# Kernel tuning notes

Hardware: AMD Instinct MI355X
Metric: run time of the kernel (lower is better)

The kernel has to match this reference:

```python
import jax, jax.numpy as jnp
import numpy as np

N_EMBD = 1024
N_HEAD = 16


def setup_inputs() -> dict:
    key = jax.random.key(0)
    k1, k2, k3, k4, k5 = jax.random.split(key, 5)
    B, T, C = 4, 2048, N_EMBD
    s = 1.0 / np.sqrt(C)
    x = jax.random.normal(k1, (B, T, C), dtype=jnp.float32)
    w_weight = jax.random.normal(k2, (3 * C, C), dtype=jnp.float32) * s
    w_bias = jax.random.normal(k3, (3 * C,), dtype=jnp.float32) * s
    proj_weight = jax.random.normal(k4, (C, C), dtype=jnp.float32) * s
    proj_bias = jax.random.normal(k5, (C,), dtype=jnp.float32) * s
    return {"x": x, "w_weight": w_weight, "w_bias": w_bias,
            "proj_weight": proj_weight, "proj_bias": proj_bias}


def reference(x, w_weight, w_bias, proj_weight, proj_bias):
    B, T, C = x.shape
    nh = N_HEAD
    hs = C // nh
    # fused QKV projection (torch Linear: x @ W^T + b)
    wei = jnp.einsum('btc,oc->bto', x, w_weight) + w_bias
    k, q, v = jnp.split(wei, 3, axis=-1)  # note: chunk order is k, q, v
    # [B, T, nh, hs] -> [B, nh, T, hs]
    key_ = k.reshape(B, T, nh, hs).transpose(0, 2, 1, 3)
    query = q.reshape(B, T, nh, hs).transpose(0, 2, 1, 3)
    value = v.reshape(B, T, nh, hs).transpose(0, 2, 1, 3)
    scale = hs ** (-0.5)
    weight = jnp.einsum('bhqd,bhkd->bhqk', query, key_) * scale
    weight = jax.nn.softmax(weight, axis=-1)
    out = jnp.einsum('bhqk,bhkd->bhqd', weight, value)  # [B, nh, T, hs]
    # Faithful to source bug: transpose(1,2) is discarded; view is taken on
    # the (B, nh, T, hs) layout directly.
    out = out.reshape(B, T, C)
    out = jnp.einsum('btc,oc->bto', out, proj_weight) + proj_bias
    return out
```

## Files before the change

kernel.cpp:

```cpp
#include <hip/hip_runtime.h>
#include <hip/hip_bf16.h>


typedef __attribute__((ext_vector_type(8)))  short bf16x8;
typedef __attribute__((ext_vector_type(4)))  float f32x4;
typedef __attribute__((ext_vector_type(16))) float f32x16;
typedef __attribute__((ext_vector_type(2)))  unsigned u32x2;

typedef __attribute__((address_space(3))) unsigned lds_u32_t;
typedef __attribute__((address_space(1))) unsigned glb_u32_t;

__device__ __forceinline__ void async_cp16(const short* g, short* l) {
    __builtin_amdgcn_global_load_lds((glb_u32_t*)g, (lds_u32_t*)l, 16, 0, 0);
}

__device__ __forceinline__ float exp2fast(float x) {
    return __builtin_amdgcn_exp2f(x);
}

__device__ __forceinline__ short f2bf(float f) {
    union { float f; unsigned u; } v; v.f = f;
    unsigned r = v.u + 0x7fffu + ((v.u >> 16) & 1u);
    return (short)(r >> 16);
}

__device__ __forceinline__ unsigned cvt_pk_bf16(float lo, float hi) {
    unsigned r;
    asm("v_cvt_pk_bf16_f32 %0, %1, %2" : "=v"(r) : "v"(lo), "v"(hi));
    return r;
}

__global__ __launch_bounds__(256) void cvt3_kernel(
    const float4* __restrict__ x,  const float4* __restrict__ ww,
    const float4* __restrict__ pw, short4* __restrict__ xb,
    short4* __restrict__ wwb,      short4* __restrict__ pwb) {
    const int b = blockIdx.x;
    const float4* in; short4* out; int i;
    if (b < 8192)       { in = x;  out = xb;  i = b * 256 + threadIdx.x; }
    else if (b < 11264) { in = ww; out = wwb; i = (b - 8192) * 256 + threadIdx.x; }
    else                { in = pw; out = pwb; i = (b - 11264) * 256 + threadIdx.x; }
    float4 v = in[i];
    short4 o;
    o.x = f2bf(v.x); o.y = f2bf(v.y); o.z = f2bf(v.z); o.w = f2bf(v.w);
    out[i] = o;
}

template<int EPI>
__global__ __launch_bounds__(256) void gemm_bf16(
    const short* __restrict__ A, const short* __restrict__ W,
    const float* __restrict__ bias, float* __restrict__ outF,
    short* __restrict__ kout, short* __restrict__ qout, short* __restrict__ vtout,
    int M, int N, int K)
{
    __shared__ short lA[2][128 * 64];
    __shared__ short lB[2][128 * 64];
    const int tid  = threadIdx.x;
    const int lane = tid & 63;
    const int wave = tid >> 6;
    const int wM = (wave >> 1) * 64;
    const int wN = (wave & 1) * 64;
    const int l15 = lane & 15, l4 = lane >> 4;
    const int rsw = (lane & 7) << 3;
    const int rowBase = blockIdx.y * 128;
    const int colBase = blockIdx.x * 128;

    auto STAGE = [&](int t, int buf) {
        const int k0 = t * 64;
        #pragma unroll
        for (int i = 0; i < 4; ++i) {
            int idx = i * 256 + tid;
            int r   = idx >> 3;
            int cp  = ((idx & 7) ^ (r & 7)) * 8;
            int eo  = idx * 8;
            async_cp16(A + (size_t)(rowBase + r) * K + k0 + cp, &lA[buf][eo]);
            async_cp16(W + (size_t)(colBase + r) * K + k0 + cp, &lB[buf][eo]);
        }
    };

    f32x4 acc[4][4] = {};
    const int NT = K >> 6;

    STAGE(0, 0);
    __syncthreads();

    int cur = 0;
    for (int t = 0; t < NT; ++t) {
        if (t + 1 < NT) STAGE(t + 1, cur ^ 1);
        #pragma unroll
        for (int kt = 0; kt < 2; ++kt) {
            bf16x8 af[4], bfr[4];
            #pragma unroll
            for (int mt = 0; mt < 4; ++mt)
                af[mt] = *(const bf16x8*)(
                    &lA[cur][(wM + mt * 16 + l15) * 64 + ((kt * 32 + l4 * 8) ^ rsw)]);
            #pragma unroll
            for (int nt = 0; nt < 4; ++nt)
                bfr[nt] = *(const bf16x8*)(
                    &lB[cur][(wN + nt * 16 + l15) * 64 + ((kt * 32 + l4 * 8) ^ rsw)]);
            #pragma unroll
            for (int mt = 0; mt < 4; ++mt)
                #pragma unroll
                for (int nt = 0; nt < 4; ++nt)
                    acc[mt][nt] = __builtin_amdgcn_mfma_f32_16x16x32_bf16(
                        af[mt], bfr[nt], acc[mt][nt], 0, 0, 0);
        }
        __syncthreads();
        cur ^= 1;
    }

    #pragma unroll
    for (int mt = 0; mt < 4; ++mt) {
        #pragma unroll
        for (int nt = 0; nt < 4; ++nt) {
            const int n  = colBase + wN + nt * 16 + l15;
            const int mb = rowBase + wM + mt * 16 + l4 * 4;
            const float bv = bias[n];
            #pragma unroll
            for (int r = 0; r < 4; ++r) {
                const int m = mb + r;
                float val = acc[mt][nt][r] + bv;
                if (EPI == 0) {
                    int b = m >> 11, t = m & 2047;
                    int j = n >> 10, hd = n & 1023;
                    int h = hd >> 6, d = hd & 63;
                    size_t base = ((size_t)(b * 16 + h) * 2048 + t) * 64 + d;
                    if (j == 0)      kout[base] = f2bf(val);
                    else if (j == 1) qout[base] = f2bf(val * 0.180336879f);
                    else             vtout[((size_t)(b * 16 + h) * 64 + d) * 2048 + t] = f2bf(val);
                } else {
                    outF[(size_t)m * N + n] = val;
                }
            }
        }
    }
}

__global__ __launch_bounds__(256) void attn_kernel(
    const short* __restrict__ Q, const short* __restrict__ Km,
    const short* __restrict__ Vt, short* __restrict__ O)
{
    __shared__ short kbuf[2][64 * 64];
    __shared__ short vbuf[2][64 * 64];

    const int tid  = threadIdx.x;
    const int lane = tid & 63;
    const int wave = tid >> 6;
    const int l31 = lane & 31;
    const int l1  = lane >> 5;

    const int b     = blockIdx.x;
    const int xcd   = b & 7;
    const int inner = b >> 3;
    const int bx    = inner & 15;
    const int bh    = xcd * 8 + (inner >> 4);
    const int q0    = bx * 128 + wave * 32;

    const short* Qh = Q  + (size_t)bh * 2048 * 64;
    const short* Kh = Km + (size_t)bh * 2048 * 64;
    const short* Vh = Vt + (size_t)bh * 64 * 2048;

    const int i8 = lane >> 3, i7 = lane & 7;
    const int srcCol = 8 * (i7 ^ i8);
    const int rsw    = (l31 & 7) << 3;

    const short* src[4];
    short* dst0[4];
    int step;
    if (wave < 2) {
        #pragma unroll
        for (int c = 0; c < 4; ++c) {
            int j = wave * 4 + c;
            src[c]  = Kh + (size_t)(8 * j + i8) * 64 + srcCol;
            dst0[c] = &kbuf[0][j * 512 + lane * 8];
        }
        step = 64 * 64;
    } else {
        #pragma unroll
        for (int c = 0; c < 4; ++c) {
            int j = (wave - 2) * 4 + c;
            src[c]  = Vh + (size_t)(8 * j + i8) * 2048 + srcCol;
            dst0[c] = &vbuf[0][j * 512 + lane * 8];
        }
        step = 64;
    }
    auto STAGE = [&](int buf) {
        #pragma unroll
        for (int c = 0; c < 4; ++c) {
            async_cp16(src[c], dst0[c] + buf * 4096);
            src[c] += step;
        }
    };

    bf16x8 qf[4];
    #pragma unroll
    for (int s = 0; s < 4; ++s)
        qf[s] = *(const bf16x8*)(Qh + (size_t)(q0 + l31) * 64 + s * 16 + l1 * 8);

    union { unsigned u[4]; bf16x8 v; } onesu;
    #pragma unroll
    for (int j = 0; j < 4; ++j) onesu.u[j] = 0x3F803F80u;
    const bf16x8 onesf = onesu.v;

    f32x16 o[2] = {};
    f32x16 ol   = {};

    STAGE(0);
    __syncthreads();

    int cur = 0;
    for (int it = 0; it < 32; ++it) {
        if (it < 31) STAGE(cur ^ 1);

        f32x16 s2[2] = {};
        __builtin_amdgcn_s_setprio(1);
        #pragma unroll
        for (int t = 0; t < 2; ++t) {
            #pragma unroll
            for (int s = 0; s < 4; ++s) {
                bf16x8 kf = *(const bf16x8*)(
                    &kbuf[cur][(t * 32 + l31) * 64 + ((s * 16 + l1 * 8) ^ rsw)]);
                s2[t] = __builtin_amdgcn_mfma_f32_32x32x16_bf16(kf, qf[s], s2[t], 0, 0, 0);
            }
        }
        __builtin_amdgcn_s_setprio(0);

        #pragma unroll
        for (int t = 0; t < 2; ++t)
            #pragma unroll
            for (int i = 0; i < 16; ++i)
                s2[t][i] = exp2fast(s2[t][i]);

        bf16x8 pa[4];
        #pragma unroll
        for (int t = 0; t < 2; ++t) {
            #pragma unroll
            for (int sl = 0; sl < 2; ++sl) {
                unsigned A0 = cvt_pk_bf16(s2[t][8 * sl + 0], s2[t][8 * sl + 1]);
                unsigned A1 = cvt_pk_bf16(s2[t][8 * sl + 2], s2[t][8 * sl + 3]);
                unsigned B0 = cvt_pk_bf16(s2[t][8 * sl + 4], s2[t][8 * sl + 5]);
                unsigned B1 = cvt_pk_bf16(s2[t][8 * sl + 6], s2[t][8 * sl + 7]);
                u32x2 ra = __builtin_amdgcn_permlane32_swap(A0, B0, false, false);
                u32x2 rb = __builtin_amdgcn_permlane32_swap(A1, B1, false, false);
                union { unsigned u[4]; bf16x8 v; } w;
                w.u[0] = ra.x;
                w.u[1] = rb.x;
                w.u[2] = ra.y;
                w.u[3] = rb.y;
                pa[2 * t + sl] = w.v;
            }
        }

        __builtin_amdgcn_s_setprio(1);
        #pragma unroll
        for (int s = 0; s < 4; ++s) {
            #pragma unroll
            for (int dt = 0; dt < 2; ++dt) {
                bf16x8 vf = *(const bf16x8*)(
                    &vbuf[cur][(dt * 32 + l31) * 64 + ((s * 16 + l1 * 8) ^ rsw)]);
                o[dt] = __builtin_amdgcn_mfma_f32_32x32x16_bf16(pa[s], vf, o[dt], 0, 0, 0);
            }
            ol = __builtin_amdgcn_mfma_f32_32x32x16_bf16(pa[s], onesf, ol, 0, 0, 0);
        }
        __builtin_amdgcn_s_setprio(0);

        __syncthreads();
        cur ^= 1;
    }

    #pragma unroll
    for (int g = 0; g < 4; ++g)
        #pragma unroll
        for (int rr = 0; rr < 4; ++rr) {
            float invl = 1.f / ol[g * 4 + rr];
            int qrow = q0 + rr + 8 * g + 4 * l1;
            size_t base = ((size_t)bh * 2048 + qrow) * 64 + l31;
            O[base]      = f2bf(o[0][g * 4 + rr] * invl);
            O[base + 32] = f2bf(o[1][g * 4 + rr] * invl);
        }
}

extern "C" void kernel_launch(void* const* d_in, const int* in_sizes, int n_in,
                              void* d_out, int out_size, void* d_ws, size_t ws_size,
                              hipStream_t stream) {
    const float* x  = (const float*)d_in[0];
    const float* ww = (const float*)d_in[1];
    const float* wb = (const float*)d_in[2];
    const float* pwt = (const float*)d_in[3];
    const float* pb  = (const float*)d_in[4];
    float* out = (float*)d_out;

    short* ws  = (short*)d_ws;
    short* xb  = ws;
    short* wwb = xb  + 8192 * 1024;
    short* pwb = wwb + 3072 * 1024;
    short* qb  = pwb + 1024 * 1024;
    short* kb  = qb  + 64 * 2048 * 64;
    short* vtb = kb  + 64 * 2048 * 64;
    short* ob  = vtb + 64 * 2048 * 64;

    cvt3_kernel<<<12288, 256, 0, stream>>>(
        (const float4*)x, (const float4*)ww, (const float4*)pwt,
        (short4*)xb, (short4*)wwb, (short4*)pwb);

    gemm_bf16<0><<<dim3(24, 64), 256, 0, stream>>>(
        xb, wwb, wb, nullptr, kb, qb, vtb, 8192, 3072, 1024);

    attn_kernel<<<1024, 256, 0, stream>>>(qb, kb, vtb, ob);

    gemm_bf16<1><<<dim3(8, 64), 256, 0, stream>>>(
        ob, pwb, pb, out, nullptr, nullptr, nullptr, 8192, 1024, 1024);
}
```

Baseline: 215.5 us.

## Restructure bf16 GEMM into 8-wave 256x128 tiles with half-K ping-pong pipeline

The GEMM now runs 512 threads (8 waves) per block over 256x128 output tiles, splitting each 64-wide K step into two 32-wide halves staged separately. Loads for the next half are issued while the current half's MFMAs run, using explicit vmcnt/lgkmcnt waits, raw s_barrier, sched_barrier and setprio. The aim is to hide global-to-LDS latency and raise MFMA issue density. In exchange there are more barriers per K step, fewer blocks in the grid (768 and 256), and more LDS pressure per block.

```diff
diff --git a/kernel.cpp b/kernel.cpp
--- a/kernel.cpp
+++ b/kernel.cpp
@@ -46,87 +46,115 @@
 }
 
 template<int EPI>
-__global__ __launch_bounds__(256) void gemm_bf16(
+__global__ __launch_bounds__(512) void gemm_bf16(
     const short* __restrict__ A, const short* __restrict__ W,
     const float* __restrict__ bias, float* __restrict__ outF,
     short* __restrict__ kout, short* __restrict__ qout, short* __restrict__ vtout,
     int M, int N, int K)
 {
-    __shared__ short lA[2][128 * 64];
-    __shared__ short lB[2][128 * 64];
+    __shared__ short lA[2][2][256 * 32];
+    __shared__ short lB[2][2][128 * 32];
     const int tid  = threadIdx.x;
     const int lane = tid & 63;
     const int wave = tid >> 6;
-    const int wM = (wave >> 1) * 64;
-    const int wN = (wave & 1) * 64;
+    const int wr = wave >> 1;
+    const int wc = wave & 1;
     const int l15 = lane & 15, l4 = lane >> 4;
-    const int rsw = (lane & 7) << 3;
-    const int rowBase = blockIdx.y * 128;
+    const int rowBase = blockIdx.y * 256;
     const int colBase = blockIdx.x * 128;
 
-    auto STAGE = [&](int t, int buf) {
-        const int k0 = t * 64;
-        #pragma unroll
-        for (int i = 0; i < 4; ++i) {
-            int idx = i * 256 + tid;
-            int r   = idx >> 3;
-            int cp  = ((idx & 7) ^ (r & 7)) * 8;
-            int eo  = idx * 8;
-            async_cp16(A + (size_t)(rowBase + r) * K + k0 + cp, &lA[buf][eo]);
-            async_cp16(W + (size_t)(colBase + r) * K + k0 + cp, &lB[buf][eo]);
-        }
+    const int ca0 = tid, ca1 = tid + 512;
+    const int ra0 = ca0 >> 2, ra1 = ca1 >> 2, rb = tid >> 2;
+    const int sa0 = ((ca0 & 3) ^ (ra0 & 3)) * 8;
+    const int sa1 = ((ca1 & 3) ^ (ra1 & 3)) * 8;
+    const int sb  = ((tid & 3) ^ (rb  & 3)) * 8;
+
+    auto STAGE_A = [&](int t, int kh) {
+        const short* base = A + (size_t)rowBase * K + t * 64 + kh * 32;
+        const int buf = t & 1;
+        async_cp16(base + (size_t)ra0 * K + sa0, &lA[buf][kh][ca0 * 8]);
+        async_cp16(base + (size_t)ra1 * K + sa1, &lA[buf][kh][ca1 * 8]);
+    };
+    auto STAGE_B = [&](int t, int kh) {
+        const short* base = W + (size_t)colBase * K + t * 64 + kh * 32;
+        const int buf = t & 1;
+        async_cp16(base + (size_t)rb * K + sb, &lB[buf][kh][tid * 8]);
     };
 
     f32x4 acc[4][4] = {};
+
+    auto READ = [&](int buf, int kh, bf16x8* af, bf16x8* bfr) {
+        #pragma unroll
+        for (int mt = 0; mt < 4; ++mt) {
+            int row = wr * 64 + mt * 16 + l15;
+            af[mt] = *(const bf16x8*)(&lA[buf][kh][row * 32 + ((l4 ^ (row & 3)) * 8)]);
+        }
+        #pragma unroll
+        for (int nt = 0; nt < 4; ++nt) {
+            int row = wc * 64 + nt * 16 + l15;
+            bfr[nt] = *(const bf16x8*)(&lB[buf][kh][row * 32 + ((l4 ^ (row & 3)) * 8)]);
+        }
+    };
+    auto MFMA16 = [&](bf16x8* af, bf16x8* bfr) {
+        #pragma unroll
+        for (int mt = 0; mt < 4; ++mt)
+            #pragma unroll
+            for (int nt = 0; nt < 4; ++nt)
+                acc[mt][nt] = __builtin_amdgcn_mfma_f32_16x16x32_bf16(
+                    af[mt], bfr[nt], acc[mt][nt], 0, 0, 0);
+    };
+
     const int NT = K >> 6;
 
-    STAGE(0, 0);
-    __syncthreads();
-
-    int cur = 0;
+    STAGE_A(0, 0); STAGE_B(0, 0);
+    STAGE_A(0, 1); STAGE_B(0, 1);
+    STAGE_A(1, 0); STAGE_B(1, 0);
+    asm volatile("s_waitcnt vmcnt(3)" ::: "memory");
+    __builtin_amdgcn_s_barrier();
+
     for (int t = 0; t < NT; ++t) {
-        if (t + 1 < NT) STAGE(t + 1, cur ^ 1);
-        #pragma unroll
-        for (int kt = 0; kt < 2; ++kt) {
-            bf16x8 af[4], bfr[4];
-            #pragma unroll
-            for (int mt = 0; mt < 4; ++mt)
-                af[mt] = *(const bf16x8*)(
-                    &lA[cur][(wM + mt * 16 + l15) * 64 + ((kt * 32 + l4 * 8) ^ rsw)]);
-            #pragma unroll
-            for (int nt = 0; nt < 4; ++nt)
-                bfr[nt] = *(const bf16x8*)(
-                    &lB[cur][(wN + nt * 16 + l15) * 64 + ((kt * 32 + l4 * 8) ^ rsw)]);
-            #pragma unroll
-            for (int mt = 0; mt < 4; ++mt)
-                #pragma unroll
-                for (int nt = 0; nt < 4; ++nt)
-                    acc[mt][nt] = __builtin_amdgcn_mfma_f32_16x16x32_bf16(
-                        af[mt], bfr[nt], acc[mt][nt], 0, 0, 0);
-        }
-        __syncthreads();
-        cur ^= 1;
+        const int buf = t & 1;
+        bf16x8 af[4], bfr[4];
+        READ(buf, 0, af, bfr);
+        if (t + 1 < NT) { STAGE_A(t + 1, 1); STAGE_B(t + 1, 1); }
+        __builtin_amdgcn_s_barrier();
+        asm volatile("s_waitcnt lgkmcnt(0)" ::: "memory");
+        __builtin_amdgcn_sched_barrier(0);
+        __builtin_amdgcn_s_setprio(1);
+        MFMA16(af, bfr);
+        __builtin_amdgcn_s_setprio(0);
+        __builtin_amdgcn_s_barrier();
+        READ(buf, 1, af, bfr);
+        if (t + 2 < NT) { STAGE_A(t + 2, 0); STAGE_B(t + 2, 0); }
+        asm volatile("s_waitcnt vmcnt(3)" ::: "memory");
+        __builtin_amdgcn_s_barrier();
+        asm volatile("s_waitcnt lgkmcnt(0)" ::: "memory");
+        __builtin_amdgcn_sched_barrier(0);
+        __builtin_amdgcn_s_setprio(1);
+        MFMA16(af, bfr);
+        __builtin_amdgcn_s_setprio(0);
+        __builtin_amdgcn_s_barrier();
     }
 
     #pragma unroll
     for (int mt = 0; mt < 4; ++mt) {
         #pragma unroll
         for (int nt = 0; nt < 4; ++nt) {
-            const int n  = colBase + wN + nt * 16 + l15;
-            const int mb = rowBase + wM + mt * 16 + l4 * 4;
+            const int n  = colBase + wc * 64 + nt * 16 + l15;
+            const int mb = rowBase + wr * 64 + mt * 16 + l4 * 4;
             const float bv = bias[n];
             #pragma unroll
             for (int r = 0; r < 4; ++r) {
                 const int m = mb + r;
                 float val = acc[mt][nt][r] + bv;
                 if (EPI == 0) {
-                    int b = m >> 11, t = m & 2047;
+                    int b = m >> 11, tt = m & 2047;
                     int j = n >> 10, hd = n & 1023;
                     int h = hd >> 6, d = hd & 63;
-                    size_t base = ((size_t)(b * 16 + h) * 2048 + t) * 64 + d;
+                    size_t base = ((size_t)(b * 16 + h) * 2048 + tt) * 64 + d;
                     if (j == 0)      kout[base] = f2bf(val);
                     else if (j == 1) qout[base] = f2bf(val * 0.180336879f);
-                    else             vtout[((size_t)(b * 16 + h) * 64 + d) * 2048 + t] = f2bf(val);
+                    else             vtout[((size_t)(b * 16 + h) * 64 + d) * 2048 + tt] = f2bf(val);
                 } else {
                     outF[(size_t)m * N + n] = val;
                 }
@@ -302,11 +330,11 @@
         (const float4*)x, (const float4*)ww, (const float4*)pwt,
         (short4*)xb, (short4*)wwb, (short4*)pwb);
 
-    gemm_bf16<0><<<dim3(24, 64), 256, 0, stream>>>(
+    gemm_bf16<0><<<dim3(24, 32), 512, 0, stream>>>(
         xb, wwb, wb, nullptr, kb, qb, vtb, 8192, 3072, 1024);
 
     attn_kernel<<<1024, 256, 0, stream>>>(qb, kb, vtb, ob);
 
-    gemm_bf16<1><<<dim3(8, 64), 256, 0, stream>>>(
+    gemm_bf16<1><<<dim3(8, 32), 512, 0, stream>>>(
         ob, pwb, pb, out, nullptr, nullptr, nullptr, 8192, 1024, 1024);
 }
```

Measured after the change: 233.8 us. 8.5% more time.
